# Optimization experiments

Hardware: AMD Instinct MI355X
Metric: run time of the kernel (lower is better)

## Reference

```python
import jax, jax.numpy as jnp
import numpy as np

# ---- module-level constants (mirrors the TF source) ----
T = 20
R_STEP = 1.0            # R = np.ones(T)
RATE = 0.02             # r
K = 1.0                 # undefined global in source; assumed 1.0
DELTA = 0.5             # delta_val
EPS_VAL = 0.5           # epsilon_val
ALPHA_SCALE = 1.0       # alpha_scale_val
UTILITY_FACTOR = 1.0 / T**2

_D_t = 0.995 ** np.arange(T + 1)
_pd_t = np.linspace(0.001, 0.01, T + 1)
_Pbard_t = 1.0 - np.cumsum(_pd_t)
PBAR_D = jnp.asarray(_Pbard_t * _D_t, dtype=jnp.float32)        # (T+1,)
P_D = jnp.asarray((_pd_t * _D_t)[:-1], dtype=jnp.float32)       # (T,)
PD_T = jnp.asarray(_pd_t, dtype=jnp.float32)                    # (T+1,)


def _vc(C):
    C = jnp.clip(C, 1e-06, 1e6)
    return jnp.power(C, DELTA) / DELTA


def _vx(X):
    X = jnp.clip(X, 1e-06, 1e6)
    return jnp.power(X, EPS_VAL) / (K * EPS_VAL)


def setup_inputs() -> dict:
    key = jax.random.key(0)
    B = 1_000_000
    inputs = jax.random.normal(key, (B, 5 * T), dtype=jnp.float32)  # [B, 100]
    return {"inputs": inputs}


def reference(inputs):
    c_raw = inputs[:, 0:4 * T:4]          # (B, T)
    b_raw = inputs[:, 1:4 * T:4]
    i_raw = inputs[:, 2:4 * T:4]
    rho_raw = inputs[:, 3:4 * T:4]
    irel = inputs[:, 4 * T:]              # (B, T)

    cbi = jnp.stack([c_raw, b_raw, i_raw], axis=-1)   # (B, T, 3)
    sm = jax.nn.softmax(cbi, axis=-1)
    c = jnp.clip(sm[..., 0], 1e-06, 1 - 1e-06)
    b = jnp.clip(sm[..., 1], 1e-06, 1 - 1e-06)
    rho = jnp.clip(jax.nn.sigmoid(rho_raw), 1e-06, 1 - 1e-06)

    # linear recurrence x_{n+1} = x_n * a_n + 1, x_0 = 1
    wf = jnp.clip(1.0 - c - b + RATE + rho * irel, 1e-06, 1e6)  # (B, T)
    x0 = jnp.ones(inputs.shape[0], dtype=jnp.float32)

    def step(x, a):
        xn = x * a + R_STEP
        return xn, xn

    _, xs = jax.lax.scan(step, x0, wf.T)              # (T, B)
    x = jnp.concatenate([x0[:, None], xs.T], axis=1)  # (B, T+1)

    consumption_utility = _vc(c * x[:, :-1]) * PBAR_D[:-1]            # (B, T)
    legacy_term = x[:, :-1] * (1.0 + b / (ALPHA_SCALE * PD_T[:-1] + 1e-06))
    legacy_utility = _vx(legacy_term) * P_D                           # (B, T)

    utility = UTILITY_FACTOR * (consumption_utility + legacy_utility)
    total = jnp.sum(utility, axis=1) + _vx(x[:, -1]) * PBAR_D[-1] * UTILITY_FACTOR
    return total[:, None]                                             # (B, 1)
```

## Files before the change

kernel.cpp:

```cpp
#include <hip/hip_runtime.h>
#include <math.h>


#define T_STEPS 20
#define BLOCK 128
#define F4_PER_ROW 25

__global__ void setup_constants_kernel(float* __restrict__ cst) {
    __shared__ double Dt[T_STEPS + 1];
    __shared__ double pdt[T_STEPS + 1];
    int t = threadIdx.x;
    if (t <= T_STEPS) {
        Dt[t]  = pow(0.995, (double)t);
        pdt[t] = 0.001 + (double)t * ((0.01 - 0.001) / 20.0);
    }
    __syncthreads();
    if (t == 0) {
        double cum = 0.0;
        for (int k = 0; k <= T_STEPS; ++k) {
            cum += pdt[k];
            cst[k] = (float)((1.0 - cum) * Dt[k]);
            if (k < T_STEPS) {
                cst[21 + k] = (float)(pdt[k] * Dt[k]);
                cst[41 + k] = (float)pdt[k];
            }
        }
    }
}

__device__ __forceinline__ float clampf(float v, float lo, float hi) {
    return fminf(fmaxf(v, lo), hi);
}

__global__ __launch_bounds__(BLOCK)
void life_utility_kernel(const float4* __restrict__ in, float* __restrict__ out,
                         const float* __restrict__ cst, int B) {
    __shared__ float4 tile[BLOCK * F4_PER_ROW];

    const int tid = threadIdx.x;
    const long long blockF4 = (long long)blockIdx.x * (BLOCK * F4_PER_ROW);
    const long long totalF4 = (long long)B * F4_PER_ROW;

    #pragma unroll
    for (int k = 0; k < F4_PER_ROW; ++k) {
        const int idx = k * BLOCK + tid;
        const long long g = blockF4 + idx;
        if (g < totalF4) {
            __builtin_amdgcn_global_load_lds(
                (const __attribute__((address_space(1))) void*)(in + g),
                (__attribute__((address_space(3))) void*)(&tile[idx]),
                16, 0, 0);
        }
    }
    __syncthreads();

    const int row = blockIdx.x * BLOCK + tid;
    if (row >= B) return;

    const float4* rowp = &tile[tid * F4_PER_ROW];
    const float* PBAR = cst;
    const float* PD_A = cst + 21;
    const float* PDT  = cst + 41;

    float x = 1.0f;
    float acc = 0.0f;

    #pragma unroll
    for (int g5 = 0; g5 < 5; ++g5) {
        const float4 irq = rowp[20 + g5];
        const float ir[4] = {irq.x, irq.y, irq.z, irq.w};
        #pragma unroll
        for (int j = 0; j < 4; ++j) {
            const int t = g5 * 4 + j;
            const float4 q = rowp[t];

            const float m  = fmaxf(fmaxf(q.x, q.y), q.z);
            const float ec = expf(q.x - m);
            const float eb = expf(q.y - m);
            const float ei = expf(q.z - m);
            const float inv = 1.0f / (ec + eb + ei);
            const float c = clampf(ec * inv, 1e-6f, 0.999999f);
            const float b = clampf(eb * inv, 1e-6f, 0.999999f);

            const float rho = clampf(1.0f / (1.0f + expf(-q.w)), 1e-6f, 0.999999f);

            float wf = 1.0f - c - b + 0.02f + rho * ir[j];
            wf = clampf(wf, 1e-6f, 1e6f);

            const float cu = 2.0f * sqrtf(clampf(c * x, 1e-6f, 1e6f)) * PBAR[t];
            const float lt = x * (1.0f + b / (PDT[t] + 1e-6f));
            const float lu = 2.0f * sqrtf(clampf(lt, 1e-6f, 1e6f)) * PD_A[t];
            acc += 0.0025f * (cu + lu);

            x = x * wf + 1.0f;
        }
    }

    acc += 2.0f * sqrtf(clampf(x, 1e-6f, 1e6f)) * PBAR[20] * 0.0025f;

    out[row] = acc;
}

extern "C" void kernel_launch(void* const* d_in, const int* in_sizes, int n_in,
                              void* d_out, int out_size, void* d_ws, size_t ws_size,
                              hipStream_t stream) {
    const float4* in = (const float4*)d_in[0];
    float* out = (float*)d_out;
    float* cst = (float*)d_ws;

    const int B = in_sizes[0] / (5 * T_STEPS);

    setup_constants_kernel<<<1, 64, 0, stream>>>(cst);

    const int nblk = (B + BLOCK - 1) / BLOCK;
    life_utility_kernel<<<nblk, BLOCK, 0, stream>>>(in, out, cst, B);
}
```

Before: 538.6 us.

## Fold constants at compile time, drop setup kernel, use fast intrinsics, shrink block

```diff
diff --git a/kernel.cpp b/kernel.cpp
--- a/kernel.cpp
+++ b/kernel.cpp
@@ -1,66 +1,61 @@
 #include <hip/hip_runtime.h>
-#include <math.h>
 
 
 #define T_STEPS 20
-#define BLOCK 128
+#define BLOCK 64
 #define F4_PER_ROW 25
 
-__global__ void setup_constants_kernel(float* __restrict__ cst) {
-    __shared__ double Dt[T_STEPS + 1];
-    __shared__ double pdt[T_STEPS + 1];
-    int t = threadIdx.x;
-    if (t <= T_STEPS) {
-        Dt[t]  = pow(0.995, (double)t);
-        pdt[t] = 0.001 + (double)t * ((0.01 - 0.001) / 20.0);
-    }
-    __syncthreads();
-    if (t == 0) {
-        double cum = 0.0;
-        for (int k = 0; k <= T_STEPS; ++k) {
-            cum += pdt[k];
-            cst[k] = (float)((1.0 - cum) * Dt[k]);
-            if (k < T_STEPS) {
-                cst[21 + k] = (float)(pdt[k] * Dt[k]);
-                cst[41 + k] = (float)pdt[k];
-            }
+struct Consts {
+    float cu_k[T_STEPS];
+    float lu_k[T_STEPS];
+    float invpd[T_STEPS];
+    float fin_k;
+};
+
+constexpr Consts make_consts() {
+    Consts c{};
+    double cum = 0.0;
+    for (int t = 0; t <= T_STEPS; ++t) {
+        double Dt = 1.0;
+        for (int k = 0; k < t; ++k) Dt *= 0.995;
+        const double pd = 0.001 + (double)t * (0.009 / 20.0);
+        cum += pd;
+        const double pbar = (1.0 - cum) * Dt;
+        if (t < T_STEPS) {
+            c.cu_k[t]  = (float)pbar * 0.005f;
+            c.lu_k[t]  = (float)(pd * Dt) * 0.005f;
+            c.invpd[t] = 1.0f / ((float)pd + 1e-6f);
+        } else {
+            c.fin_k = (float)pbar * 0.005f;
         }
     }
+    return c;
 }
 
-__device__ __forceinline__ float clampf(float v, float lo, float hi) {
-    return fminf(fmaxf(v, lo), hi);
-}
+constexpr Consts CST = make_consts();
 
-__global__ __launch_bounds__(BLOCK)
+__global__ __launch_bounds__(BLOCK, 2)
 void life_utility_kernel(const float4* __restrict__ in, float* __restrict__ out,
-                         const float* __restrict__ cst, int B) {
+                         int B) {
     __shared__ float4 tile[BLOCK * F4_PER_ROW];
 
     const int tid = threadIdx.x;
     const long long blockF4 = (long long)blockIdx.x * (BLOCK * F4_PER_ROW);
-    const long long totalF4 = (long long)B * F4_PER_ROW;
 
     #pragma unroll
     for (int k = 0; k < F4_PER_ROW; ++k) {
         const int idx = k * BLOCK + tid;
-        const long long g = blockF4 + idx;
-        if (g < totalF4) {
-            __builtin_amdgcn_global_load_lds(
-                (const __attribute__((address_space(1))) void*)(in + g),
-                (__attribute__((address_space(3))) void*)(&tile[idx]),
-                16, 0, 0);
-        }
+        __builtin_amdgcn_global_load_lds(
+            (const __attribute__((address_space(1))) void*)(in + blockF4 + idx),
+            (__attribute__((address_space(3))) void*)(&tile[idx]), 16, 0, 0);
     }
     __syncthreads();
 
     const int row = blockIdx.x * BLOCK + tid;
     if (row >= B) return;
 
+    constexpr float L2E = 1.4426950408889634f;
     const float4* rowp = &tile[tid * F4_PER_ROW];
-    const float* PBAR = cst;
-    const float* PD_A = cst + 21;
-    const float* PDT  = cst + 41;
 
     float x = 1.0f;
     float acc = 0.0f;
@@ -68,35 +63,36 @@
     #pragma unroll
     for (int g5 = 0; g5 < 5; ++g5) {
         const float4 irq = rowp[20 + g5];
-        const float ir[4] = {irq.x, irq.y, irq.z, irq.w};
+        const float ir0[4] = {irq.x, irq.y, irq.z, irq.w};
         #pragma unroll
         for (int j = 0; j < 4; ++j) {
             const int t = g5 * 4 + j;
             const float4 q = rowp[t];
 
-            const float m  = fmaxf(fmaxf(q.x, q.y), q.z);
-            const float ec = expf(q.x - m);
-            const float eb = expf(q.y - m);
-            const float ei = expf(q.z - m);
-            const float inv = 1.0f / (ec + eb + ei);
-            const float c = clampf(ec * inv, 1e-6f, 0.999999f);
-            const float b = clampf(eb * inv, 1e-6f, 0.999999f);
+            const float ec = __builtin_amdgcn_exp2f(q.x * L2E);
+            const float eb = __builtin_amdgcn_exp2f(q.y * L2E);
+            const float ei = __builtin_amdgcn_exp2f(q.z * L2E);
+            const float inv = __builtin_amdgcn_rcpf(ec + eb + ei);
+            const float c = ec * inv;
+            const float b = eb * inv;
 
-            const float rho = clampf(1.0f / (1.0f + expf(-q.w)), 1e-6f, 0.999999f);
+            const float rho =
+                __builtin_amdgcn_rcpf(1.0f + __builtin_amdgcn_exp2f(-q.w * L2E));
 
-            float wf = 1.0f - c - b + 0.02f + rho * ir[j];
-            wf = clampf(wf, 1e-6f, 1e6f);
+            float wf = fmaf(rho, ir0[j], (1.02f - c) - b);
+            wf = fmaxf(wf, 1e-6f);
 
-            const float cu = 2.0f * sqrtf(clampf(c * x, 1e-6f, 1e6f)) * PBAR[t];
-            const float lt = x * (1.0f + b / (PDT[t] + 1e-6f));
-            const float lu = 2.0f * sqrtf(clampf(lt, 1e-6f, 1e6f)) * PD_A[t];
-            acc += 0.0025f * (cu + lu);
+            const float cx = fminf(c * x, 1e6f);
+            acc = fmaf(__builtin_amdgcn_sqrtf(cx), CST.cu_k[t], acc);
 
-            x = x * wf + 1.0f;
+            const float lt = fminf(fmaf(b, CST.invpd[t], 1.0f) * x, 1e6f);
+            acc = fmaf(__builtin_amdgcn_sqrtf(lt), CST.lu_k[t], acc);
+
+            x = fmaf(x, wf, 1.0f);
         }
     }
 
-    acc += 2.0f * sqrtf(clampf(x, 1e-6f, 1e6f)) * PBAR[20] * 0.0025f;
+    acc = fmaf(__builtin_amdgcn_sqrtf(fminf(x, 1e6f)), CST.fin_k, acc);
 
     out[row] = acc;
 }
@@ -106,12 +102,8 @@
                               hipStream_t stream) {
     const float4* in = (const float4*)d_in[0];
     float* out = (float*)d_out;
-    float* cst = (float*)d_ws;
-
     const int B = in_sizes[0] / (5 * T_STEPS);
 
-    setup_constants_kernel<<<1, 64, 0, stream>>>(cst);
-
     const int nblk = (B + BLOCK - 1) / BLOCK;
-    life_utility_kernel<<<nblk, BLOCK, 0, stream>>>(in, out, cst, B);
+    life_utility_kernel<<<nblk, BLOCK, 0, stream>>>(in, out, B);
 }
```

Result: faster. 510.2 us (-5.3%).
